# Kernel tuning notes

Hardware: AMD Instinct MI355X
Metric: run time of the kernel (lower is better)

## Reference

```python
import jax, jax.numpy as jnp
from jax import lax
import numpy as np

SEQ, B, IN, H = 512, 64, 1024, 1024


def setup_inputs() -> dict:
    key = jax.random.key(0)
    ks = jax.random.split(key, 9)
    s = 0.02
    return {
        "x":   jax.random.normal(ks[0], (SEQ, B, IN), dtype=jnp.float32),
        # layer 0: Linear(input_dim, hidden) and Linear(hidden, hidden)
        "Wi0": jax.random.normal(ks[1], (H, IN), dtype=jnp.float32) * s,
        "bi0": jax.random.normal(ks[2], (H,), dtype=jnp.float32) * s,
        "Wh0": jax.random.normal(ks[3], (H, H), dtype=jnp.float32) * s,
        "bh0": jax.random.normal(ks[4], (H,), dtype=jnp.float32) * s,
        # layer 1: Linear(hidden, hidden) twice
        "Wi1": jax.random.normal(ks[5], (H, H), dtype=jnp.float32) * s,
        "bi1": jax.random.normal(ks[6], (H,), dtype=jnp.float32) * s,
        "Wh1": jax.random.normal(ks[7], (H, H), dtype=jnp.float32) * s,
        "bh1": jax.random.normal(ks[8], (H,), dtype=jnp.float32) * s,
    }


def reference(x, Wi0, bi0, Wh0, bh0, Wi1, bi1, Wh1, bh1):
    # x: [seq, batch, in]; two-layer tanh RNN, time-major, zero initial hidden.
    batch = x.shape[1]
    hdim = Wh0.shape[0]
    h0 = jnp.zeros((2, batch, hdim), dtype=x.dtype)

    def step(h_prev, x_t):
        h1 = jnp.tanh(x_t @ Wi0.T + bi0 + h_prev[0] @ Wh0.T + bh0)
        h2 = jnp.tanh(h1 @ Wi1.T + bi1 + h_prev[1] @ Wh1.T + bh1)
        return jnp.stack([h1, h2], axis=0), h2

    h_final, outputs = lax.scan(step, h0, x)
    return outputs, h_final
```

## Files before the change

### kernel.cpp

```cpp
#include <hip/hip_runtime.h>


#define SEQ 512
#define BATCH 64
#define HID 1024
#define BH (BATCH * HID)

typedef __attribute__((ext_vector_type(8))) short short8;
typedef __attribute__((ext_vector_type(4))) float f32x4;
typedef __attribute__((ext_vector_type(4))) unsigned int u32x4;

__device__ __forceinline__ unsigned short f32_to_bf16_rne(float f) {
    unsigned int u = __float_as_uint(f);
    u += 0x7FFFu + ((u >> 16) & 1u);
    return (unsigned short)(u >> 16);
}

__device__ __forceinline__ short8 cvt8(float4 f0, float4 f1) {
    short8 w;
    w[0] = (short)f32_to_bf16_rne(f0.x);
    w[1] = (short)f32_to_bf16_rne(f0.y);
    w[2] = (short)f32_to_bf16_rne(f0.z);
    w[3] = (short)f32_to_bf16_rne(f0.w);
    w[4] = (short)f32_to_bf16_rne(f1.x);
    w[5] = (short)f32_to_bf16_rne(f1.y);
    w[6] = (short)f32_to_bf16_rne(f1.z);
    w[7] = (short)f32_to_bf16_rne(f1.w);
    return w;
}

__device__ __forceinline__ void ld_cc16(short8& d, const unsigned short* p) {
    asm volatile("global_load_dwordx4 %0, %1, off sc0 sc1"
                 : "=v"(d) : "v"(p) : "memory");
}

__device__ __forceinline__ void vm_wait0() {
    asm volatile("s_waitcnt vmcnt(0)" ::: "memory");
    __builtin_amdgcn_sched_barrier(0);
}

__device__ __forceinline__ unsigned long long pack4_bf16(float a, float b, float c, float d) {
    return (unsigned long long)f32_to_bf16_rne(a)
         | ((unsigned long long)f32_to_bf16_rne(b) << 16)
         | ((unsigned long long)f32_to_bf16_rne(c) << 32)
         | ((unsigned long long)f32_to_bf16_rne(d) << 48);
}

__device__ __forceinline__ int poll_min64(const unsigned int* f) {
    u32x4 r[16];
    #pragma unroll
    for (int i = 0; i < 16; ++i)
        asm volatile("global_load_dwordx4 %0, %1, off sc0 sc1"
                     : "=v"(r[i]) : "v"(f + i * 4) : "memory");
    asm volatile("s_waitcnt vmcnt(0)" ::: "memory");
    __builtin_amdgcn_sched_barrier(0);
    unsigned mn = r[0][0];
    #pragma unroll
    for (int i = 0; i < 16; ++i)
        #pragma unroll
        for (int j = 0; j < 4; ++j)
            mn = mn < r[i][j] ? mn : r[i][j];
    return (int)mn;
}

__device__ __forceinline__ void wait_min64(const unsigned int* f, int target) {
    if (target <= 0) return;
    while (poll_min64(f) < target) __builtin_amdgcn_s_sleep(1);
}

__global__ void cvt_f32_bf16(const float* __restrict__ src,
                             unsigned short* __restrict__ dst, int n4) {
    int i = blockIdx.x * blockDim.x + threadIdx.x;
    int stride = gridDim.x * blockDim.x;
    for (; i < n4; i += stride) {
        float4 f = ((const float4*)src)[i];
        ushort4 o;
        o.x = f32_to_bf16_rne(f.x);
        o.y = f32_to_bf16_rne(f.y);
        o.z = f32_to_bf16_rne(f.z);
        o.w = f32_to_bf16_rne(f.w);
        ((ushort4*)dst)[i] = o;
    }
}

__global__ void init_ws(uint4* __restrict__ p, int n16) {
    int i = blockIdx.x * blockDim.x + threadIdx.x;
    if (i < n16) p[i] = make_uint4(0u, 0u, 0u, 0u);
}

#define MFMA16(W, A, ACC) \
    ACC = __builtin_amdgcn_mfma_f32_16x16x32_bf16((W), (A), (ACC), 0, 0, 0)

__global__ __launch_bounds__(256, 1) void rnn_mfma(
    const float* __restrict__ x,
    const unsigned short* __restrict__ xb, int use_xb,
    const float* __restrict__ Wi0, const float* __restrict__ bi0,
    const float* __restrict__ Wh0, const float* __restrict__ bh0,
    const float* __restrict__ Wi1, const float* __restrict__ bi1,
    const float* __restrict__ Wh1, const float* __restrict__ bh1,
    float* __restrict__ out,
    unsigned short* __restrict__ rings,
    unsigned int* __restrict__ flags)
{
    unsigned short* h1ring = rings;
    unsigned short* h2ring = rings + 4 * BH;

    const int tid   = threadIdx.x;
    const int wg    = blockIdx.x;
    const int layer = wg >> 7;
    const int m_blk = (wg >> 6) & 1;
    const int n_blk = wg & 63;
    const int wv    = tid >> 6;
    const int lane  = tid & 63;
    const int src   = wv >> 1;
    const int kh    = wv & 1;
    const int koff  = kh * 512;

    unsigned int* grpL0 = flags + (0 * 2 + m_blk) * 64;
    unsigned int* grpL1 = flags + (1 * 2 + m_blk) * 64;
    unsigned int* ep_self = (layer ? grpL1 : grpL0) + n_blk;

    const float* Wsel = layer ? (src ? Wh1 : Wi1) : (src ? Wh0 : Wi0);
    const int f_w  = n_blk * 16 + (lane & 15);
    const int kcb  = koff + (lane >> 4) * 8;
    short8 wreg[16];
    {
        const float* rw = Wsel + (size_t)f_w * HID + kcb;
        #pragma unroll
        for (int ks = 0; ks < 16; ++ks)
            wreg[ks] = cvt8(*(const float4*)(rw + ks * 32),
                            *(const float4*)(rw + ks * 32 + 4));
    }

    const int arow0 = m_blk * 32 + (lane & 15);
    const int arow1 = arow0 + 16;
    const size_t aoff0 = (size_t)arow0 * HID + kcb;
    const size_t aoff1 = (size_t)arow1 * HID + kcb;

    const int r_row = tid & 31;
    const int r_fg  = (tid >> 5) & 3;
    const int nb    = n_blk * 16 + r_fg * 4;
    const int rg    = m_blk * 32 + r_row;
    const float* biv = layer ? bi1 : bi0;
    const float* bhv = layer ? bh1 : bh0;
    float bias4[4];
    #pragma unroll
    for (int j = 0; j < 4; ++j) bias4[j] = biv[nb + j] + bhv[nb + j];

    __shared__ float red[4][16][33];

    for (int s = 0; s < SEQ; ++s) {
        f32x4 acc0 = {0.f, 0.f, 0.f, 0.f};
        f32x4 acc1 = {0.f, 0.f, 0.f, 0.f};

        if (layer == 0 && src == 0) {
            if (use_xb) {
                const unsigned short* px = xb + (size_t)s * BH;
                #pragma unroll
                for (int ks = 0; ks < 16; ++ks) {
                    short8 a0 = *(const short8*)(px + aoff0 + ks * 32);
                    short8 a1 = *(const short8*)(px + aoff1 + ks * 32);
                    MFMA16(wreg[ks], a0, acc0);
                    MFMA16(wreg[ks], a1, acc1);
                }
            } else {
                const float* px = x + (size_t)s * BH;
                #pragma unroll
                for (int ks = 0; ks < 16; ++ks) {
                    short8 a0 = cvt8(*(const float4*)(px + aoff0 + ks * 32),
                                     *(const float4*)(px + aoff0 + ks * 32 + 4));
                    short8 a1 = cvt8(*(const float4*)(px + aoff1 + ks * 32),
                                     *(const float4*)(px + aoff1 + ks * 32 + 4));
                    MFMA16(wreg[ks], a0, acc0);
                    MFMA16(wreg[ks], a1, acc1);
                }
            }
        } else {
            const unsigned short* pr;
            if (layer == 0) {
                if (lane == 0) {
                    wait_min64(grpL0, s);
                    wait_min64(grpL1, s - 3);
                }
                pr = h1ring + (size_t)((s - 1) & 3) * BH;
            } else if (src == 1) {
                if (lane == 0) wait_min64(grpL1, s);
                pr = h2ring + (size_t)((s - 1) & 3) * BH;
            } else {
                if (lane == 0) wait_min64(grpL0, s + 1);
                pr = h1ring + (size_t)(s & 3) * BH;
            }
            #pragma unroll
            for (int c = 0; c < 2; ++c) {
                short8 a0[8], a1[8];
                #pragma unroll
                for (int k = 0; k < 8; ++k) {
                    ld_cc16(a0[k], pr + aoff0 + (c * 8 + k) * 32);
                    ld_cc16(a1[k], pr + aoff1 + (c * 8 + k) * 32);
                }
                vm_wait0();
                #pragma unroll
                for (int k = 0; k < 8; ++k) {
                    MFMA16(wreg[c * 8 + k], a0[k], acc0);
                    MFMA16(wreg[c * 8 + k], a1[k], acc1);
                }
            }
        }

        #pragma unroll
        for (int r = 0; r < 4; ++r) {
            red[wv][4 * (lane >> 4) + r][lane & 15]      = acc0[r];
            red[wv][4 * (lane >> 4) + r][16 + (lane & 15)] = acc1[r];
        }
        __syncthreads();

        float v[4];
        if (tid < 128) {
            #pragma unroll
            for (int j = 0; j < 4; ++j) {
                const int ff = r_fg * 4 + j;
                float sum = red[0][ff][r_row] + red[1][ff][r_row]
                          + red[2][ff][r_row] + red[3][ff][r_row] + bias4[j];
                v[j] = tanhf(sum);
            }
            unsigned short* ring_self =
                (layer ? h2ring : h1ring) + (size_t)(s & 3) * BH;
            __hip_atomic_store((unsigned long long*)(ring_self + (size_t)rg * HID + nb),
                               pack4_bf16(v[0], v[1], v[2], v[3]),
                               __ATOMIC_RELAXED, __HIP_MEMORY_SCOPE_AGENT);
        }

        asm volatile("s_waitcnt vmcnt(0)" ::: "memory");
        __syncthreads();
        if (tid == 0)
            __hip_atomic_store(ep_self, (unsigned)(s + 1),
                               __ATOMIC_RELAXED, __HIP_MEMORY_SCOPE_AGENT);

        if (tid < 128) {
            if (layer == 1) {
                *(float4*)(out + (size_t)s * BH + (size_t)rg * HID + nb) =
                    make_float4(v[0], v[1], v[2], v[3]);
                if (s == SEQ - 1)
                    *(float4*)(out + (size_t)SEQ * BH + BH + (size_t)rg * HID + nb) =
                        make_float4(v[0], v[1], v[2], v[3]);
            } else if (s == SEQ - 1) {
                *(float4*)(out + (size_t)SEQ * BH + (size_t)rg * HID + nb) =
                    make_float4(v[0], v[1], v[2], v[3]);
            }
        }
    }
}

extern "C" void kernel_launch(void* const* d_in, const int* in_sizes, int n_in,
                              void* d_out, int out_size, void* d_ws, size_t ws_size,
                              hipStream_t stream) {
    const float* xp   = (const float*)d_in[0];
    const float* Wi0p = (const float*)d_in[1];
    const float* bi0p = (const float*)d_in[2];
    const float* Wh0p = (const float*)d_in[3];
    const float* bh0p = (const float*)d_in[4];
    const float* Wi1p = (const float*)d_in[5];
    const float* bi1p = (const float*)d_in[6];
    const float* Wh1p = (const float*)d_in[7];
    const float* bh1p = (const float*)d_in[8];
    float* outp = (float*)d_out;

    unsigned short* rings = (unsigned short*)d_ws;
    const size_t ring_bytes = (size_t)8 * BH * sizeof(unsigned short);
    unsigned int* flags = (unsigned int*)((char*)d_ws + ring_bytes);
    const size_t flag_pad = 4096;
    unsigned short* xb = (unsigned short*)((char*)d_ws + ring_bytes + flag_pad);
    const size_t xb_bytes = (size_t)SEQ * BH * 2;
    const int use_xb = (ws_size >= ring_bytes + flag_pad + xb_bytes) ? 1 : 0;

    {
        const int n16 = (int)((ring_bytes + flag_pad) / 16);
        init_ws<<<(n16 + 255) / 256, 256, 0, stream>>>((uint4*)d_ws, n16);
    }
    if (use_xb)
        cvt_f32_bf16<<<2048, 256, 0, stream>>>(xp, xb, SEQ * BH / 4);

    rnn_mfma<<<dim3(256), dim3(256), 0, stream>>>(
        xp, xb, use_xb,
        Wi0p, bi0p, Wh0p, bh0p, Wi1p, bi1p, Wh1p, bh1p,
        outp, rings, flags);
}
```

Before: 4.520 ms.

## Repartition RNN into 64 larger workgroups with both weight matrices per wave

Restructures the persistent RNN kernel from 256 workgroups of 256 threads to 64 workgroups of 512 threads. Each wave now holds both the input and recurrent weight tiles in registers and covers 64 output features instead of 16. This cuts the number of flag-polling peers from 64 to 16 and overlaps the x-projection with the wait in layer 0. The ring depth grows from 4 to 8 to give more slack between layers. In exchange, each wave does twice the MFMA work per step, layer 1 now runs its two matmuls serially within a wave, and the doubled weight registers risk pressure or spills.

```diff
diff --git a/kernel.cpp b/kernel.cpp
--- a/kernel.cpp
+++ b/kernel.cpp
@@ -5,6 +5,7 @@
 #define BATCH 64
 #define HID 1024
 #define BH (BATCH * HID)
+#define DEPTH 8
 
 typedef __attribute__((ext_vector_type(8))) short short8;
 typedef __attribute__((ext_vector_type(4))) float f32x4;
@@ -46,26 +47,26 @@
          | ((unsigned long long)f32_to_bf16_rne(d) << 48);
 }
 
-__device__ __forceinline__ int poll_min64(const unsigned int* f) {
-    u32x4 r[16];
+__device__ __forceinline__ int poll_min16(const unsigned int* f) {
+    u32x4 r[4];
     #pragma unroll
-    for (int i = 0; i < 16; ++i)
+    for (int i = 0; i < 4; ++i)
         asm volatile("global_load_dwordx4 %0, %1, off sc0 sc1"
                      : "=v"(r[i]) : "v"(f + i * 4) : "memory");
     asm volatile("s_waitcnt vmcnt(0)" ::: "memory");
     __builtin_amdgcn_sched_barrier(0);
     unsigned mn = r[0][0];
     #pragma unroll
-    for (int i = 0; i < 16; ++i)
+    for (int i = 0; i < 4; ++i)
         #pragma unroll
         for (int j = 0; j < 4; ++j)
             mn = mn < r[i][j] ? mn : r[i][j];
     return (int)mn;
 }
 
-__device__ __forceinline__ void wait_min64(const unsigned int* f, int target) {
+__device__ __forceinline__ void wait_min16(const unsigned int* f, int target) {
     if (target <= 0) return;
-    while (poll_min64(f) < target) __builtin_amdgcn_s_sleep(1);
+    while (poll_min16(f) < target) __builtin_amdgcn_s_sleep(1);
 }
 
 __global__ void cvt_f32_bf16(const float* __restrict__ src,
@@ -91,7 +92,7 @@
 #define MFMA16(W, A, ACC) \
     ACC = __builtin_amdgcn_mfma_f32_16x16x32_bf16((W), (A), (ACC), 0, 0, 0)
 
-__global__ __launch_bounds__(256, 1) void rnn_mfma(
+__global__ __launch_bounds__(512, 1) void rnn_mfma(
     const float* __restrict__ x,
     const unsigned short* __restrict__ xb, int use_xb,
     const float* __restrict__ Wi0, const float* __restrict__ bi0,
@@ -103,33 +104,37 @@
     unsigned int* __restrict__ flags)
 {
     unsigned short* h1ring = rings;
-    unsigned short* h2ring = rings + 4 * BH;
+    unsigned short* h2ring = rings + DEPTH * BH;
 
     const int tid   = threadIdx.x;
     const int wg    = blockIdx.x;
-    const int layer = wg >> 7;
-    const int m_blk = (wg >> 6) & 1;
-    const int n_blk = wg & 63;
+    const int layer = wg >> 5;
+    const int m_blk = (wg >> 4) & 1;
+    const int n_blk = wg & 15;
     const int wv    = tid >> 6;
     const int lane  = tid & 63;
-    const int src   = wv >> 1;
+    const int fg    = wv >> 1;
     const int kh    = wv & 1;
-    const int koff  = kh * 512;
 
     unsigned int* grpL0 = flags + (0 * 2 + m_blk) * 64;
     unsigned int* grpL1 = flags + (1 * 2 + m_blk) * 64;
     unsigned int* ep_self = (layer ? grpL1 : grpL0) + n_blk;
 
-    const float* Wsel = layer ? (src ? Wh1 : Wi1) : (src ? Wh0 : Wi0);
-    const int f_w  = n_blk * 16 + (lane & 15);
-    const int kcb  = koff + (lane >> 4) * 8;
-    short8 wreg[16];
+    const int f_w = n_blk * 64 + fg * 16 + (lane & 15);
+    const int kcb = kh * 512 + (lane >> 4) * 8;
+    const float* WA = layer ? Wi1 : Wi0;
+    const float* WB = layer ? Wh1 : Wh0;
+    short8 wregA[16], wregB[16];
     {
-        const float* rw = Wsel + (size_t)f_w * HID + kcb;
+        const float* ra = WA + (size_t)f_w * HID + kcb;
+        const float* rb = WB + (size_t)f_w * HID + kcb;
         #pragma unroll
-        for (int ks = 0; ks < 16; ++ks)
-            wreg[ks] = cvt8(*(const float4*)(rw + ks * 32),
-                            *(const float4*)(rw + ks * 32 + 4));
+        for (int ks = 0; ks < 16; ++ks) {
+            wregA[ks] = cvt8(*(const float4*)(ra + ks * 32),
+                             *(const float4*)(ra + ks * 32 + 4));
+            wregB[ks] = cvt8(*(const float4*)(rb + ks * 32),
+                             *(const float4*)(rb + ks * 32 + 4));
+        }
     }
 
     const int arow0 = m_blk * 32 + (lane & 15);
@@ -138,8 +143,8 @@
     const size_t aoff1 = (size_t)arow1 * HID + kcb;
 
     const int r_row = tid & 31;
-    const int r_fg  = (tid >> 5) & 3;
-    const int nb    = n_blk * 16 + r_fg * 4;
+    const int r_f4  = tid >> 5;
+    const int nb    = n_blk * 64 + r_f4 * 4;
     const int rg    = m_blk * 32 + r_row;
     const float* biv = layer ? bi1 : bi0;
     const float* bhv = layer ? bh1 : bh0;
@@ -147,21 +152,21 @@
     #pragma unroll
     for (int j = 0; j < 4; ++j) bias4[j] = biv[nb + j] + bhv[nb + j];
 
-    __shared__ float red[4][16][33];
+    __shared__ float red[8][16][33];
 
     for (int s = 0; s < SEQ; ++s) {
         f32x4 acc0 = {0.f, 0.f, 0.f, 0.f};
         f32x4 acc1 = {0.f, 0.f, 0.f, 0.f};
 
-        if (layer == 0 && src == 0) {
+        if (layer == 0) {
             if (use_xb) {
                 const unsigned short* px = xb + (size_t)s * BH;
                 #pragma unroll
                 for (int ks = 0; ks < 16; ++ks) {
                     short8 a0 = *(const short8*)(px + aoff0 + ks * 32);
                     short8 a1 = *(const short8*)(px + aoff1 + ks * 32);
-                    MFMA16(wreg[ks], a0, acc0);
-                    MFMA16(wreg[ks], a1, acc1);
+                    MFMA16(wregA[ks], a0, acc0);
+                    MFMA16(wregA[ks], a1, acc1);
                 }
             } else {
                 const float* px = x + (size_t)s * BH;
@@ -171,25 +176,16 @@
                                      *(const float4*)(px + aoff0 + ks * 32 + 4));
                     short8 a1 = cvt8(*(const float4*)(px + aoff1 + ks * 32),
                                      *(const float4*)(px + aoff1 + ks * 32 + 4));
-                    MFMA16(wreg[ks], a0, acc0);
-                    MFMA16(wreg[ks], a1, acc1);
-                }
-            }
-        } else {
-            const unsigned short* pr;
-            if (layer == 0) {
-                if (lane == 0) {
-                    wait_min64(grpL0, s);
-                    wait_min64(grpL1, s - 3);
-                }
-                pr = h1ring + (size_t)((s - 1) & 3) * BH;
-            } else if (src == 1) {
-                if (lane == 0) wait_min64(grpL1, s);
-                pr = h2ring + (size_t)((s - 1) & 3) * BH;
-            } else {
-                if (lane == 0) wait_min64(grpL0, s + 1);
-                pr = h1ring + (size_t)(s & 3) * BH;
-            }
+                    MFMA16(wregA[ks], a0, acc0);
+                    MFMA16(wregA[ks], a1, acc1);
+                }
+            }
+            if (tid == 0) {
+                wait_min16(grpL1, s - (DEPTH - 1));
+                wait_min16(grpL0, s);
+            }
+            __syncthreads();
+            const unsigned short* pr = h1ring + (size_t)((s - 1) & (DEPTH - 1)) * BH;
             #pragma unroll
             for (int c = 0; c < 2; ++c) {
                 short8 a0[8], a1[8];
@@ -201,30 +197,69 @@
                 vm_wait0();
                 #pragma unroll
                 for (int k = 0; k < 8; ++k) {
-                    MFMA16(wreg[c * 8 + k], a0[k], acc0);
-                    MFMA16(wreg[c * 8 + k], a1[k], acc1);
+                    MFMA16(wregB[c * 8 + k], a0[k], acc0);
+                    MFMA16(wregB[c * 8 + k], a1[k], acc1);
+                }
+            }
+        } else {
+            if (tid == 0) wait_min16(grpL1, s);
+            __syncthreads();
+            const unsigned short* pr2 = h2ring + (size_t)((s - 1) & (DEPTH - 1)) * BH;
+            #pragma unroll
+            for (int c = 0; c < 2; ++c) {
+                short8 a0[8], a1[8];
+                #pragma unroll
+                for (int k = 0; k < 8; ++k) {
+                    ld_cc16(a0[k], pr2 + aoff0 + (c * 8 + k) * 32);
+                    ld_cc16(a1[k], pr2 + aoff1 + (c * 8 + k) * 32);
+                }
+                vm_wait0();
+                #pragma unroll
+                for (int k = 0; k < 8; ++k) {
+                    MFMA16(wregB[c * 8 + k], a0[k], acc0);
+                    MFMA16(wregB[c * 8 + k], a1[k], acc1);
+                }
+            }
+            if (tid == 0) wait_min16(grpL0, s + 1);
+            __syncthreads();
+            const unsigned short* pr1 = h1ring + (size_t)(s & (DEPTH - 1)) * BH;
+            #pragma unroll
+            for (int c = 0; c < 2; ++c) {
+                short8 a0[8], a1[8];
+                #pragma unroll
+                for (int k = 0; k < 8; ++k) {
+                    ld_cc16(a0[k], pr1 + aoff0 + (c * 8 + k) * 32);
+                    ld_cc16(a1[k], pr1 + aoff1 + (c * 8 + k) * 32);
+                }
+                vm_wait0();
+                #pragma unroll
+                for (int k = 0; k < 8; ++k) {
+                    MFMA16(wregA[c * 8 + k], a0[k], acc0);
+                    MFMA16(wregA[c * 8 + k], a1[k], acc1);
                 }
             }
         }
 
         #pragma unroll
         for (int r = 0; r < 4; ++r) {
-            red[wv][4 * (lane >> 4) + r][lane & 15]      = acc0[r];
+            red[wv][4 * (lane >> 4) + r][lane & 15]        = acc0[r];
             red[wv][4 * (lane >> 4) + r][16 + (lane & 15)] = acc1[r];
         }
         __syncthreads();
 
         float v[4];
-        if (tid < 128) {
+        {
             #pragma unroll
             for (int j = 0; j < 4; ++j) {
-                const int ff = r_fg * 4 + j;
-                float sum = red[0][ff][r_row] + red[1][ff][r_row]
-                          + red[2][ff][r_row] + red[3][ff][r_row] + bias4[j];
+                const int f   = r_f4 * 4 + j;
+                const int fgi = f >> 4;
+                const int ff  = f & 15;
+                float sum = red[2 * fgi][ff][r_row] + red[2 * fgi + 1][ff][r_row]
+                          + bias4[j];
                 v[j] = tanhf(sum);
             }
             unsigned short* ring_self =
-                (layer ? h2ring : h1ring) + (size_t)(s & 3) * BH;
+                (layer ? h2ring : h1ring) + (size_t)(s & (DEPTH - 1)) * BH;
             __hip_atomic_store((unsigned long long*)(ring_self + (size_t)rg * HID + nb),
                                pack4_bf16(v[0], v[1], v[2], v[3]),
                                __ATOMIC_RELAXED, __HIP_MEMORY_SCOPE_AGENT);
@@ -236,17 +271,15 @@
             __hip_atomic_store(ep_self, (unsigned)(s + 1),
                                __ATOMIC_RELAXED, __HIP_MEMORY_SCOPE_AGENT);
 
-        if (tid < 128) {
-            if (layer == 1) {
-                *(float4*)(out + (size_t)s * BH + (size_t)rg * HID + nb) =
+        if (layer == 1) {
+            *(float4*)(out + (size_t)s * BH + (size_t)rg * HID + nb) =
+                make_float4(v[0], v[1], v[2], v[3]);
+            if (s == SEQ - 1)
+                *(float4*)(out + (size_t)SEQ * BH + BH + (size_t)rg * HID + nb) =
                     make_float4(v[0], v[1], v[2], v[3]);
-                if (s == SEQ - 1)
-                    *(float4*)(out + (size_t)SEQ * BH + BH + (size_t)rg * HID + nb) =
-                        make_float4(v[0], v[1], v[2], v[3]);
-            } else if (s == SEQ - 1) {
-                *(float4*)(out + (size_t)SEQ * BH + (size_t)rg * HID + nb) =
-                    make_float4(v[0], v[1], v[2], v[3]);
-            }
+        } else if (s == SEQ - 1) {
+            *(float4*)(out + (size_t)SEQ * BH + (size_t)rg * HID + nb) =
+                make_float4(v[0], v[1], v[2], v[3]);
         }
     }
 }
@@ -266,7 +299,7 @@
     float* outp = (float*)d_out;
 
     unsigned short* rings = (unsigned short*)d_ws;
-    const size_t ring_bytes = (size_t)8 * BH * sizeof(unsigned short);
+    const size_t ring_bytes = (size_t)2 * DEPTH * BH * sizeof(unsigned short);
     unsigned int* flags = (unsigned int*)((char*)d_ws + ring_bytes);
     const size_t flag_pad = 4096;
     unsigned short* xb = (unsigned short*)((char*)d_ws + ring_bytes + flag_pad);
@@ -280,7 +313,7 @@
     if (use_xb)
         cvt_f32_bf16<<<2048, 256, 0, stream>>>(xp, xb, SEQ * BH / 4);
 
-    rnn_mfma<<<dim3(256), dim3(256), 0, stream>>>(
+    rnn_mfma<<<dim3(64), dim3(512), 0, stream>>>(
         xp, xb, use_xb,
         Wi0p, bi0p, Wh0p, bh0p, Wi1p, bi1p, Wh1p, bh1p,
         outp, rings, flags);
```

Result: slower. 8.861 ms (+96.1%).

## Deepen hidden-state rings, shrink flags to 16-bit, pipeline ring loads

Applied to the files above, without the earlier changes.

Increases the ring buffer depth from 4 to 8 so layer 0 can run further ahead of layer 1, and shrinks per-block progress flags to 16-bit so each poll needs half the loads. It fuses the two flag polls in layer 0 into one combined wait, and restructures the recurrent-input matmul into a double-buffered load/MFMA pipeline that uses partial vmcnt waits instead of full drains. These changes target inter-block synchronisation latency and load stalls on the serial critical path. The trade-offs are more workspace, and 16-bit flags that are fine for 512 steps but would wrap on longer sequences.

```diff
diff --git a/kernel.cpp b/kernel.cpp
--- a/kernel.cpp
+++ b/kernel.cpp
@@ -5,6 +5,7 @@
 #define BATCH 64
 #define HID 1024
 #define BH (BATCH * HID)
+#define DEPTH 8
 
 typedef __attribute__((ext_vector_type(8))) short short8;
 typedef __attribute__((ext_vector_type(4))) float f32x4;
@@ -38,6 +39,15 @@
     asm volatile("s_waitcnt vmcnt(0)" ::: "memory");
     __builtin_amdgcn_sched_barrier(0);
 }
+__device__ __forceinline__ void vm_wait8() {
+    asm volatile("s_waitcnt vmcnt(8)" ::: "memory");
+    __builtin_amdgcn_sched_barrier(0);
+}
+
+__device__ __forceinline__ void st_ep16(unsigned short* p, unsigned v) {
+    asm volatile("global_store_short %0, %1, off sc0 sc1"
+                 :: "v"(p), "v"(v) : "memory");
+}
 
 __device__ __forceinline__ unsigned long long pack4_bf16(float a, float b, float c, float d) {
     return (unsigned long long)f32_to_bf16_rne(a)
@@ -46,26 +56,97 @@
          | ((unsigned long long)f32_to_bf16_rne(d) << 48);
 }
 
-__device__ __forceinline__ int poll_min64(const unsigned int* f) {
-    u32x4 r[16];
-    #pragma unroll
-    for (int i = 0; i < 16; ++i)
-        asm volatile("global_load_dwordx4 %0, %1, off sc0 sc1"
-                     : "=v"(r[i]) : "v"(f + i * 4) : "memory");
-    asm volatile("s_waitcnt vmcnt(0)" ::: "memory");
-    __builtin_amdgcn_sched_barrier(0);
-    unsigned mn = r[0][0];
-    #pragma unroll
-    for (int i = 0; i < 16; ++i)
-        #pragma unroll
-        for (int j = 0; j < 4; ++j)
-            mn = mn < r[i][j] ? mn : r[i][j];
-    return (int)mn;
-}
-
-__device__ __forceinline__ void wait_min64(const unsigned int* f, int target) {
+__device__ __forceinline__ unsigned min_u16x4(u32x4 w, unsigned mn) {
+    #pragma unroll
+    for (int j = 0; j < 4; ++j) {
+        unsigned lo = w[j] & 0xFFFFu, hi = w[j] >> 16;
+        mn = mn < lo ? mn : lo;
+        mn = mn < hi ? mn : hi;
+    }
+    return mn;
+}
+
+__device__ __forceinline__ void wait_one(const unsigned short* f, int target) {
     if (target <= 0) return;
-    while (poll_min64(f) < target) __builtin_amdgcn_s_sleep(1);
+    for (;;) {
+        u32x4 r[8];
+        #pragma unroll
+        for (int i = 0; i < 8; ++i)
+            asm volatile("global_load_dwordx4 %0, %1, off sc0 sc1"
+                         : "=v"(r[i]) : "v"((const unsigned int*)f + i * 4) : "memory");
+        asm volatile("s_waitcnt vmcnt(0)" ::: "memory");
+        __builtin_amdgcn_sched_barrier(0);
+        unsigned mn = 0xFFFFu;
+        #pragma unroll
+        for (int i = 0; i < 8; ++i) mn = min_u16x4(r[i], mn);
+        if ((int)mn >= target) return;
+        __builtin_amdgcn_s_sleep(1);
+    }
+}
+
+__device__ __forceinline__ void wait_two(const unsigned short* f0, int t0,
+                                         const unsigned short* f1, int t1) {
+    if (t0 <= 0 && t1 <= 0) return;
+    for (;;) {
+        u32x4 r0[8], r1[8];
+        #pragma unroll
+        for (int i = 0; i < 8; ++i)
+            asm volatile("global_load_dwordx4 %0, %1, off sc0 sc1"
+                         : "=v"(r0[i]) : "v"((const unsigned int*)f0 + i * 4) : "memory");
+        #pragma unroll
+        for (int i = 0; i < 8; ++i)
+            asm volatile("global_load_dwordx4 %0, %1, off sc0 sc1"
+                         : "=v"(r1[i]) : "v"((const unsigned int*)f1 + i * 4) : "memory");
+        asm volatile("s_waitcnt vmcnt(0)" ::: "memory");
+        __builtin_amdgcn_sched_barrier(0);
+        unsigned m0 = 0xFFFFu, m1 = 0xFFFFu;
+        #pragma unroll
+        for (int i = 0; i < 8; ++i) { m0 = min_u16x4(r0[i], m0); m1 = min_u16x4(r1[i], m1); }
+        if ((int)m0 >= t0 && (int)m1 >= t1) return;
+        __builtin_amdgcn_s_sleep(1);
+    }
+}
+
+#define MFMA16(W, A, ACC) \
+    ACC = __builtin_amdgcn_mfma_f32_16x16x32_bf16((W), (A), (ACC), 0, 0, 0)
+
+__device__ __forceinline__ void ring_mm(const unsigned short* pr,
+                                        size_t aoff0, size_t aoff1,
+                                        const short8* wreg,
+                                        f32x4& acc0, f32x4& acc1) {
+    short8 a0[4], a1[4], b0[4], b1[4];
+    #pragma unroll
+    for (int k = 0; k < 4; ++k) {
+        ld_cc16(a0[k], pr + aoff0 + k * 32);
+        ld_cc16(a1[k], pr + aoff1 + k * 32);
+    }
+    #pragma unroll
+    for (int k = 0; k < 4; ++k) {
+        ld_cc16(b0[k], pr + aoff0 + (4 + k) * 32);
+        ld_cc16(b1[k], pr + aoff1 + (4 + k) * 32);
+    }
+    vm_wait8();
+    #pragma unroll
+    for (int k = 0; k < 4; ++k) { MFMA16(wreg[k], a0[k], acc0); MFMA16(wreg[k], a1[k], acc1); }
+    #pragma unroll
+    for (int k = 0; k < 4; ++k) {
+        ld_cc16(a0[k], pr + aoff0 + (8 + k) * 32);
+        ld_cc16(a1[k], pr + aoff1 + (8 + k) * 32);
+    }
+    vm_wait8();
+    #pragma unroll
+    for (int k = 0; k < 4; ++k) { MFMA16(wreg[4 + k], b0[k], acc0); MFMA16(wreg[4 + k], b1[k], acc1); }
+    #pragma unroll
+    for (int k = 0; k < 4; ++k) {
+        ld_cc16(b0[k], pr + aoff0 + (12 + k) * 32);
+        ld_cc16(b1[k], pr + aoff1 + (12 + k) * 32);
+    }
+    vm_wait8();
+    #pragma unroll
+    for (int k = 0; k < 4; ++k) { MFMA16(wreg[8 + k], a0[k], acc0); MFMA16(wreg[8 + k], a1[k], acc1); }
+    vm_wait0();
+    #pragma unroll
+    for (int k = 0; k < 4; ++k) { MFMA16(wreg[12 + k], b0[k], acc0); MFMA16(wreg[12 + k], b1[k], acc1); }
 }
 
 __global__ void cvt_f32_bf16(const float* __restrict__ src,
@@ -88,9 +169,6 @@
     if (i < n16) p[i] = make_uint4(0u, 0u, 0u, 0u);
 }
 
-#define MFMA16(W, A, ACC) \
-    ACC = __builtin_amdgcn_mfma_f32_16x16x32_bf16((W), (A), (ACC), 0, 0, 0)
-
 __global__ __launch_bounds__(256, 1) void rnn_mfma(
     const float* __restrict__ x,
     const unsigned short* __restrict__ xb, int use_xb,
@@ -100,10 +178,10 @@
     const float* __restrict__ Wh1, const float* __restrict__ bh1,
     float* __restrict__ out,
     unsigned short* __restrict__ rings,
-    unsigned int* __restrict__ flags)
+    unsigned short* __restrict__ flags)
 {
     unsigned short* h1ring = rings;
-    unsigned short* h2ring = rings + 4 * BH;
+    unsigned short* h2ring = rings + DEPTH * BH;
 
     const int tid   = threadIdx.x;
     const int wg    = blockIdx.x;
@@ -116,9 +194,9 @@
     const int kh    = wv & 1;
     const int koff  = kh * 512;
 
-    unsigned int* grpL0 = flags + (0 * 2 + m_blk) * 64;
-    unsigned int* grpL1 = flags + (1 * 2 + m_blk) * 64;
-    unsigned int* ep_self = (layer ? grpL1 : grpL0) + n_blk;
+    unsigned short* grpL0 = flags + (0 * 2 + m_blk) * 64;
+    unsigned short* grpL1 = flags + (1 * 2 + m_blk) * 64;
+    unsigned short* ep_self = (layer ? grpL1 : grpL0) + n_blk;
 
     const float* Wsel = layer ? (src ? Wh1 : Wi1) : (src ? Wh0 : Wi0);
     const int f_w  = n_blk * 16 + (lane & 15);
@@ -178,38 +256,22 @@
         } else {
             const unsigned short* pr;
             if (layer == 0) {
-                if (lane == 0) {
-                    wait_min64(grpL0, s);
-                    wait_min64(grpL1, s - 3);
-                }
-                pr = h1ring + (size_t)((s - 1) & 3) * BH;
+                if (lane == 0)
+                    wait_two(grpL0, s, grpL1, s - (DEPTH - 1));
+                pr = h1ring + (size_t)((s - 1) & (DEPTH - 1)) * BH;
             } else if (src == 1) {
-                if (lane == 0) wait_min64(grpL1, s);
-                pr = h2ring + (size_t)((s - 1) & 3) * BH;
+                if (lane == 0) wait_one(grpL1, s);
+                pr = h2ring + (size_t)((s - 1) & (DEPTH - 1)) * BH;
             } else {
-                if (lane == 0) wait_min64(grpL0, s + 1);
-                pr = h1ring + (size_t)(s & 3) * BH;
+                if (lane == 0) wait_one(grpL0, s + 1);
+                pr = h1ring + (size_t)(s & (DEPTH - 1)) * BH;
             }
-            #pragma unroll
-            for (int c = 0; c < 2; ++c) {
-                short8 a0[8], a1[8];
-                #pragma unroll
-                for (int k = 0; k < 8; ++k) {
-                    ld_cc16(a0[k], pr + aoff0 + (c * 8 + k) * 32);
-                    ld_cc16(a1[k], pr + aoff1 + (c * 8 + k) * 32);
-                }
-                vm_wait0();
-                #pragma unroll
-                for (int k = 0; k < 8; ++k) {
-                    MFMA16(wreg[c * 8 + k], a0[k], acc0);
-                    MFMA16(wreg[c * 8 + k], a1[k], acc1);
-                }
-            }
+            ring_mm(pr, aoff0, aoff1, wreg, acc0, acc1);
         }
 
         #pragma unroll
         for (int r = 0; r < 4; ++r) {
-            red[wv][4 * (lane >> 4) + r][lane & 15]      = acc0[r];
+            red[wv][4 * (lane >> 4) + r][lane & 15]        = acc0[r];
             red[wv][4 * (lane >> 4) + r][16 + (lane & 15)] = acc1[r];
         }
         __syncthreads();
@@ -224,7 +286,7 @@
                 v[j] = tanhf(sum);
             }
             unsigned short* ring_self =
-                (layer ? h2ring : h1ring) + (size_t)(s & 3) * BH;
+                (layer ? h2ring : h1ring) + (size_t)(s & (DEPTH - 1)) * BH;
             __hip_atomic_store((unsigned long long*)(ring_self + (size_t)rg * HID + nb),
                                pack4_bf16(v[0], v[1], v[2], v[3]),
                                __ATOMIC_RELAXED, __HIP_MEMORY_SCOPE_AGENT);
@@ -233,8 +295,7 @@
         asm volatile("s_waitcnt vmcnt(0)" ::: "memory");
         __syncthreads();
         if (tid == 0)
-            __hip_atomic_store(ep_self, (unsigned)(s + 1),
-                               __ATOMIC_RELAXED, __HIP_MEMORY_SCOPE_AGENT);
+            st_ep16(ep_self, (unsigned)(s + 1));
 
         if (tid < 128) {
             if (layer == 1) {
@@ -266,8 +327,8 @@
     float* outp = (float*)d_out;
 
     unsigned short* rings = (unsigned short*)d_ws;
-    const size_t ring_bytes = (size_t)8 * BH * sizeof(unsigned short);
-    unsigned int* flags = (unsigned int*)((char*)d_ws + ring_bytes);
+    const size_t ring_bytes = (size_t)2 * DEPTH * BH * sizeof(unsigned short);
+    unsigned short* flags = (unsigned short*)((char*)d_ws + ring_bytes);
     const size_t flag_pad = 4096;
     unsigned short* xb = (unsigned short*)((char*)d_ws + ring_bytes + flag_pad);
     const size_t xb_bytes = (size_t)SEQ * BH * 2;
```

After: 5.134 ms. +13.6%, slower.
